# Kernel optimization log

Measured on AMD Instinct MI355X. Metric: run time of the kernel, lower is better.

## Reference

```python
import jax, jax.numpy as jnp
import numpy as np

B, S, H = 2, 2048, 2048
NH, NG = 16, 4           # attention heads, query groups
HD = H // NH             # head_dim = 128
HPG = NH // NG           # heads per group = 4


def setup_inputs() -> dict:
    key = jax.random.key(0)
    ks = jax.random.split(key, 8)
    s = 0.02
    return {
        "hidden_states": jax.random.normal(ks[0], (B, S, H), dtype=jnp.float32),
        "attention_mask": jnp.ones((B, S), dtype=jnp.int32),
        "Wq": jax.random.normal(ks[1], (H, H), dtype=jnp.float32) * s,
        "bq": jnp.zeros((H,), dtype=jnp.float32),
        "Wk": jax.random.normal(ks[2], (HD * NG, H), dtype=jnp.float32) * s,
        "bk": jnp.zeros((HD * NG,), dtype=jnp.float32),
        "Wv": jax.random.normal(ks[3], (HD * NG, H), dtype=jnp.float32) * s,
        "bv": jnp.zeros((HD * NG,), dtype=jnp.float32),
    }


def reference(hidden_states, attention_mask, Wq, bq, Wk, bk, Wv, bv):
    b, s, _ = hidden_states.shape
    scale = 1.0 / np.sqrt(HD).astype(np.float32)
    # projections (torch Linear: x @ W.T + b)
    q = hidden_states @ Wq.T + bq                      # [b,s,H]
    k = hidden_states @ Wk.T + bk                      # [b,s,NG*HD]
    v = hidden_states @ Wv.T + bv
    # q grouped so that repeat_interleave of k/v along heads == broadcast over heads_per_group
    q = q.reshape(b, s, NG, HPG, HD)                   # heads = group-major order
    k = k.reshape(b, s, NG, HD)
    v = v.reshape(b, s, NG, HD)
    scores = jnp.einsum("bsgpd,btgd->bgpst", q, k) * scale  # [b,NG,HPG,s,s]
    # mask: positions with attention_mask == 0 get finfo.min added
    mask_add = jnp.where(attention_mask == 0,
                         jnp.finfo(scores.dtype).min,
                         jnp.float32(0.0))             # [b,t]
    scores = scores + mask_add[:, None, None, None, :]
    attn = jax.nn.softmax(scores, axis=-1)             # dropout is identity in eval
    out = jnp.einsum("bgpst,btgd->bsgpd", attn, v)     # [b,s,NG,HPG,HD]
    return out.reshape(b, s, NH * HD)
```

## Files before the change

### kernel.cpp

```cpp
#include <hip/hip_runtime.h>
#include <hip/hip_bf16.h>

#define B_ 2
#define S_ 2048
#define H_ 2048
#define NH_ 16
#define NG_ 4
#define HD_ 128
#define HPG_ 4

typedef __attribute__((ext_vector_type(8))) short short8;
typedef __attribute__((ext_vector_type(4))) short short4v;
typedef __attribute__((ext_vector_type(4))) float float4v;

#define MFMA_BF16 __builtin_amdgcn_mfma_f32_16x16x32_bf16

#if __has_builtin(__builtin_amdgcn_exp2f)
#define EXP2(x) __builtin_amdgcn_exp2f(x)
#else
#define EXP2(x) exp2f(x)
#endif

__device__ __forceinline__ void gload16(const void* g, void* l) {
    __builtin_amdgcn_global_load_lds(
        (const __attribute__((address_space(1))) unsigned int*)g,
        (__attribute__((address_space(3))) unsigned int*)l, 16, 0, 0);
}

__device__ __forceinline__ short bf16bits(float f) {
    union { __hip_bfloat16 h; short s; } u;
    u.h = __float2bfloat16(f);
    return u.s;
}

__global__ __launch_bounds__(256) void cvt_all(const float* __restrict__ hs,
                                               const float* __restrict__ wq,
                                               const float* __restrict__ wk,
                                               const float* __restrict__ wv,
                                               const int* __restrict__ mask,
                                               __hip_bfloat16* __restrict__ o_hs,
                                               __hip_bfloat16* __restrict__ o_wq,
                                               __hip_bfloat16* __restrict__ o_wk,
                                               __hip_bfloat16* __restrict__ o_wv,
                                               float* __restrict__ o_m) {
    int i = blockIdx.x * 256 + threadIdx.x;
    if (blockIdx.x == 0) {
#pragma unroll
        for (int j = 0; j < 16; ++j) {
            int idx = threadIdx.x * 16 + j;
            o_m[idx] = mask[idx] ? 0.0f : -3.0e38f;
        }
    }
    const float* src;
    __hip_bfloat16* dst;
    int off;
    if (i < 1048576)      { src = hs; dst = o_hs; off = i; }
    else if (i < 1572864) { src = wq; dst = o_wq; off = i - 1048576; }
    else if (i < 1703936) { src = wk; dst = o_wk; off = i - 1572864; }
    else                  { src = wv; dst = o_wv; off = i - 1703936; }
    const float4* s4 = (const float4*)src;
    float4 a = s4[2 * (size_t)off];
    float4 b = s4[2 * (size_t)off + 1];
    union { short8 s; __hip_bfloat16 h[8]; } u;
    u.h[0] = __float2bfloat16(a.x); u.h[1] = __float2bfloat16(a.y);
    u.h[2] = __float2bfloat16(a.z); u.h[3] = __float2bfloat16(a.w);
    u.h[4] = __float2bfloat16(b.x); u.h[5] = __float2bfloat16(b.y);
    u.h[6] = __float2bfloat16(b.z); u.h[7] = __float2bfloat16(b.w);
    *(short8*)(dst + 8 * (size_t)off) = u.s;
}

__global__ __launch_bounds__(256) void gemm_qkv(const __hip_bfloat16* __restrict__ A,
                                                const __hip_bfloat16* __restrict__ Wq,
                                                const __hip_bfloat16* __restrict__ Wk,
                                                const __hip_bfloat16* __restrict__ Wv,
                                                const float* __restrict__ bq,
                                                const float* __restrict__ bk,
                                                const float* __restrict__ bv,
                                                __hip_bfloat16* __restrict__ qO,
                                                __hip_bfloat16* __restrict__ kO,
                                                __hip_bfloat16* __restrict__ vTO) {
    __shared__ char lds[32768];

    const int bx = blockIdx.x;
    const __hip_bfloat16* Bw;
    const float* bias;
    int bn, mode;
    if (bx < 16)      { Bw = Wq; bias = bq; bn = bx * 128;        mode = 0; }
    else if (bx < 20) { Bw = Wk; bias = bk; bn = (bx - 16) * 128; mode = 1; }
    else              { Bw = Wv; bias = bv; bn = (bx - 20) * 128; mode = 2; }

    const int tid = threadIdx.x;
    const int lane = tid & 63;
    const int x = lane & 15, g = lane >> 4;
    const int wid = tid >> 6;
    const int wm = wid >> 1, wn = wid & 1;
    const int bm = blockIdx.y * 128;
    const int K = 2048;

    const int srow = tid >> 2;
    const int schunk = (tid & 3) ^ ((tid >> 3) & 3);
    const __hip_bfloat16* gA0 = A + (size_t)(bm + srow) * K + schunk * 8;
    const __hip_bfloat16* gA1 = A + (size_t)(bm + 64 + srow) * K + schunk * 8;
    const __hip_bfloat16* gB0 = Bw + (size_t)(bn + srow) * K + schunk * 8;
    const __hip_bfloat16* gB1 = Bw + (size_t)(bn + 64 + srow) * K + schunk * 8;

    int aoff[4], boff[4];
    const int key = (x >> 1) & 3;
#pragma unroll
    for (int t = 0; t < 4; ++t) {
        aoff[t] = ((wm * 64 + t * 16 + x) * 32 + (g ^ key) * 8) * 2;
        boff[t] = 8192 + ((wn * 64 + t * 16 + x) * 32 + (g ^ key) * 8) * 2;
    }

    float4v acc[4][4];
#pragma unroll
    for (int i = 0; i < 4; ++i)
#pragma unroll
        for (int j = 0; j < 4; ++j) acc[i][j] = (float4v)0.f;

    gload16(gA0, lds + tid * 16);
    gload16(gA1, lds + tid * 16 + 4096);
    gload16(gB0, lds + 8192 + tid * 16);
    gload16(gB1, lds + 8192 + tid * 16 + 4096);
    gA0 += 32; gA1 += 32; gB0 += 32; gB1 += 32;

    for (int it = 0; it < 64; ++it) {
        char* cur = lds + (it & 1) * 16384;
        char* nxt = lds + ((it & 1) ^ 1) * 16384;
        __syncthreads();
        if (it < 63) {
            gload16(gA0, nxt + tid * 16);
            gload16(gA1, nxt + tid * 16 + 4096);
            gload16(gB0, nxt + 8192 + tid * 16);
            gload16(gB1, nxt + 8192 + tid * 16 + 4096);
            gA0 += 32; gA1 += 32; gB0 += 32; gB1 += 32;
        }
        short8 af[4], bf[4];
#pragma unroll
        for (int t = 0; t < 4; ++t) {
            af[t] = *(const short8*)(cur + aoff[t]);
            bf[t] = *(const short8*)(cur + boff[t]);
        }
#pragma unroll
        for (int mb = 0; mb < 4; ++mb)
#pragma unroll
            for (int nb = 0; nb < 4; ++nb)
                acc[mb][nb] = MFMA_BF16(af[mb], bf[nb], acc[mb][nb], 0, 0, 0);
    }

    if (mode <= 1) {
        const int N = (mode == 0) ? 2048 : 512;
        __hip_bfloat16* C = (mode == 0) ? qO : kO;
#pragma unroll
        for (int nb = 0; nb < 4; ++nb) {
            const int n = bn + wn * 64 + nb * 16 + x;
            const float bsv = bias[n];
#pragma unroll
            for (int mb = 0; mb < 4; ++mb) {
                const int m0 = bm + wm * 64 + mb * 16 + g * 4;
#pragma unroll
                for (int r = 0; r < 4; ++r)
                    C[(size_t)(m0 + r) * N + n] = __float2bfloat16(acc[mb][nb][r] + bsv);
            }
        }
    } else {
#pragma unroll
        for (int nb = 0; nb < 4; ++nb) {
            const int n = bn + wn * 64 + nb * 16 + x;
            const float bsv = bias[n];
            const int gv = n >> 7, d = n & 127;
#pragma unroll
            for (int mb = 0; mb < 4; ++mb) {
                const int m0 = bm + wm * 64 + mb * 16 + g * 4;
                const int bb = m0 >> 11, s = m0 & 2047;
                short4v pk;
#pragma unroll
                for (int r = 0; r < 4; ++r) pk[r] = bf16bits(acc[mb][nb][r] + bsv);
                *(short4v*)(vTO + ((size_t)(bb * NG_ + gv) * HD_ + d) * S_ + s) = pk;
            }
        }
    }
}

__global__ __launch_bounds__(256, 2) void attn(const __hip_bfloat16* __restrict__ q,
                                               const __hip_bfloat16* __restrict__ k,
                                               const __hip_bfloat16* __restrict__ vT,
                                               const float* __restrict__ M,
                                               float* __restrict__ out) {
    __shared__ char smem[50176];
    char* Ks = smem;
    char* Vs = smem + 16384;
    char* Ps = smem + 32768;

    const int tid = threadIdx.x;
    const int lane = tid & 63;
    const int w = tid >> 6;
    const int wm = w >> 1, wn = w & 1;
    const int x = lane & 15, g = lane >> 4;

    const int bid0 = blockIdx.x;
    const int bid = ((bid0 & 7) << 6) | (bid0 >> 3);
    const int qt = bid & 15;
    const int hp = (bid >> 4) & 3;
    const int gi = (bid >> 6) & 3;
    const int b = bid >> 8;
    const int head = gi * HPG_ + hp;
    const int q0 = qt * 128;

    short8 qf[4][4];
#pragma unroll
    for (int nb = 0; nb < 4; ++nb) {
        const int qq = q0 + wn * 64 + nb * 16 + x;
        const __hip_bfloat16* qrow = q + ((size_t)(b * S_ + qq) * NH_ + head) * HD_ + g * 8;
#pragma unroll
        for (int ks = 0; ks < 4; ++ks)
            qf[nb][ks] = *(const short8*)(qrow + ks * 32);
    }

    const int krow = tid >> 4;
    const int kchunk = (tid & 15) ^ krow;
    const __hip_bfloat16* kp = k + ((size_t)(b * S_ + krow) * NG_ + gi) * HD_ + kchunk * 8;
    const int vrow = tid >> 3;
    const int vchunk = (tid & 7) ^ (vrow & 7);
    const __hip_bfloat16* vp = vT + ((size_t)(b * NG_ + gi) * HD_ + vrow) * S_ + vchunk * 8;
    const float* mp = M + b * S_ + wm * 32 + g * 4;

    float4v O[4][4];
#pragma unroll
    for (int i = 0; i < 4; ++i)
#pragma unroll
        for (int j = 0; j < 4; ++j) O[i][j] = (float4v)0.f;
    float l_part[4] = {0.f, 0.f, 0.f, 0.f};

    const float SM = 0.08838834764831845f * 1.4426950408889634f;

#pragma unroll
    for (int qq = 0; qq < 4; ++qq)
        gload16(kp + qq * 8192, Ks + tid * 16 + qq * 4096);
    kp += 32768;

    for (int it = 0; it < 32; ++it) {
        __syncthreads();
        float4 mv0 = *(const float4*)(mp);
        float4 mv1 = *(const float4*)(mp + 16);
        mp += 64;
#pragma unroll
        for (int qq = 0; qq < 4; ++qq)
            gload16(vp + (size_t)qq * 65536, Vs + tid * 16 + qq * 4096);
        vp += 64;

        float4v sc[2][4];
#pragma unroll
        for (int i = 0; i < 2; ++i)
#pragma unroll
            for (int j = 0; j < 4; ++j) sc[i][j] = (float4v)0.f;
        __builtin_amdgcn_s_setprio(1);
#pragma unroll
        for (int ks = 0; ks < 4; ++ks) {
            short8 af0 = *(const short8*)(Ks + (wm * 32 + x) * 256 + (((ks * 4 + g) ^ x) * 16));
            short8 af1 = *(const short8*)(Ks + (wm * 32 + 16 + x) * 256 + (((ks * 4 + g) ^ x) * 16));
#pragma unroll
            for (int nb = 0; nb < 4; ++nb) {
                sc[0][nb] = MFMA_BF16(af0, qf[nb][ks], sc[0][nb], 0, 0, 0);
                sc[1][nb] = MFMA_BF16(af1, qf[nb][ks], sc[1][nb], 0, 0, 0);
            }
        }
        __builtin_amdgcn_s_setprio(0);

#pragma unroll
        for (int mb = 0; mb < 2; ++mb) {
            const float4 mv = mb ? mv1 : mv0;
            const int hs = wm * 8 + mb * 4 + g;
#pragma unroll
            for (int nb = 0; nb < 4; ++nb) {
                float p0 = EXP2(fmaf(sc[mb][nb][0], SM, mv.x));
                float p1 = EXP2(fmaf(sc[mb][nb][1], SM, mv.y));
                float p2 = EXP2(fmaf(sc[mb][nb][2], SM, mv.z));
                float p3 = EXP2(fmaf(sc[mb][nb][3], SM, mv.w));
                l_part[nb] += (p0 + p1) + (p2 + p3);
                short4v pk;
                pk[0] = bf16bits(p0); pk[1] = bf16bits(p1);
                pk[2] = bf16bits(p2); pk[3] = bf16bits(p3);
                *(short4v*)(Ps + (wn * 64 + nb * 16 + x) * 136 + hs * 8) = pk;
            }
        }

        __syncthreads();
        if (it < 31) {
#pragma unroll
            for (int qq = 0; qq < 4; ++qq)
                gload16(kp + qq * 8192, Ks + tid * 16 + qq * 4096);
            kp += 32768;
        }

#pragma unroll
        for (int ks = 0; ks < 2; ++ks) {
            short8 vf[4], pf[4];
#pragma unroll
            for (int i4 = 0; i4 < 4; ++i4) {
                vf[i4] = *(const short8*)(Vs + (wm * 64 + i4 * 16 + x) * 128 +
                                          (((ks * 4 + g) ^ (x & 7)) * 16));
                const char* pb = Ps + (wn * 64 + i4 * 16 + x) * 136 + (8 * ks + 2 * g) * 8;
                union { short4v h[2]; short8 s8; } uu;
                uu.h[0] = *(const short4v*)pb;
                uu.h[1] = *(const short4v*)(pb + 8);
                pf[i4] = uu.s8;
            }
            __builtin_amdgcn_s_setprio(1);
#pragma unroll
            for (int mb = 0; mb < 4; ++mb)
#pragma unroll
                for (int nb = 0; nb < 4; ++nb)
                    O[mb][nb] = MFMA_BF16(vf[mb], pf[nb], O[mb][nb], 0, 0, 0);
            __builtin_amdgcn_s_setprio(0);
        }
    }

    __syncthreads();
#pragma unroll
    for (int nb = 0; nb < 4; ++nb) {
        l_part[nb] += __shfl_xor(l_part[nb], 16);
        l_part[nb] += __shfl_xor(l_part[nb], 32);
    }
    float* lws = (float*)Ps;
    if (g == 0) {
#pragma unroll
        for (int nb = 0; nb < 4; ++nb)
            lws[wm * 128 + wn * 64 + nb * 16 + x] = l_part[nb];
    }
    __syncthreads();
    float inv[4];
#pragma unroll
    for (int nb = 0; nb < 4; ++nb)
        inv[nb] = 1.0f / (l_part[nb] + lws[(wm ^ 1) * 128 + wn * 64 + nb * 16 + x]);

#pragma unroll
    for (int mb = 0; mb < 4; ++mb) {
#pragma unroll
        for (int nb = 0; nb < 4; ++nb) {
            const int qq = q0 + wn * 64 + nb * 16 + x;
            const int d0 = wm * 64 + mb * 16 + g * 4;
            float4v o = O[mb][nb] * inv[nb];
            *(float4v*)(out + (size_t)(b * S_ + qq) * H_ + head * HD_ + d0) = o;
        }
    }
}

extern "C" void kernel_launch(void* const* d_in, const int* in_sizes, int n_in,
                              void* d_out, int out_size, void* d_ws, size_t ws_size,
                              hipStream_t stream) {
    (void)in_sizes; (void)n_in; (void)out_size; (void)ws_size;
    const float* hs = (const float*)d_in[0];
    const int* amask = (const int*)d_in[1];
    const float* Wq = (const float*)d_in[2];
    const float* bq = (const float*)d_in[3];
    const float* Wk = (const float*)d_in[4];
    const float* bk = (const float*)d_in[5];
    const float* Wv = (const float*)d_in[6];
    const float* bv = (const float*)d_in[7];
    float* out = (float*)d_out;

    char* ws = (char*)d_ws;
    __hip_bfloat16* hsB = (__hip_bfloat16*)(ws);
    __hip_bfloat16* WqB = (__hip_bfloat16*)(ws + 16777216);
    __hip_bfloat16* WkB = (__hip_bfloat16*)(ws + 25165824);
    __hip_bfloat16* WvB = (__hip_bfloat16*)(ws + 27262976);
    __hip_bfloat16* qB  = (__hip_bfloat16*)(ws + 29360128);
    __hip_bfloat16* kB  = (__hip_bfloat16*)(ws + 46137344);
    __hip_bfloat16* vTB = (__hip_bfloat16*)(ws + 50331648);
    float* Mf           = (float*)(ws + 54525952);

    cvt_all<<<7168, 256, 0, stream>>>(hs, Wq, Wk, Wv, amask, hsB, WqB, WkB, WvB, Mf);
    gemm_qkv<<<dim3(24, 32), 256, 0, stream>>>(hsB, WqB, WkB, WvB, bq, bk, bv, qB, kB, vTB);
    attn<<<512, 256, 0, stream>>>(qB, kB, vTB, Mf, out);
}
```

Baseline: 247.8 us.

## Rewrite QKV GEMM with 256x192 tiles, 4-stage LDS pipeline and concatenated weights

Replaces the 128x128 three-way QKV GEMM with one kernel that treats Wq/Wk/Wv as a single concatenated weight matrix (relying on their contiguous workspace layout) and uses 256x192 tiles on 512 threads. It adds a 4-stage global_load_lds ring buffer with split A/B loads, explicit vmcnt waits, barriers and setprio around the MFMA bursts, plus a swizzled block ordering for L2 reuse. Biases are concatenated in the conversion kernel. The aim is more arithmetic reuse per loaded tile and better overlap of loads with MFMA. In exchange it needs 112KB of dynamic LDS, which limits occupancy, and the hand-placed waitcnt makes correctness fragile.

```diff
diff --git a/kernel.cpp b/kernel.cpp
--- a/kernel.cpp
+++ b/kernel.cpp
@@ -38,17 +38,29 @@
                                                const float* __restrict__ wk,
                                                const float* __restrict__ wv,
                                                const int* __restrict__ mask,
+                                               const float* __restrict__ bq,
+                                               const float* __restrict__ bk,
+                                               const float* __restrict__ bv,
                                                __hip_bfloat16* __restrict__ o_hs,
                                                __hip_bfloat16* __restrict__ o_wq,
                                                __hip_bfloat16* __restrict__ o_wk,
                                                __hip_bfloat16* __restrict__ o_wv,
-                                               float* __restrict__ o_m) {
+                                               float* __restrict__ o_m,
+                                               float* __restrict__ o_bc) {
     int i = blockIdx.x * 256 + threadIdx.x;
     if (blockIdx.x == 0) {
 #pragma unroll
         for (int j = 0; j < 16; ++j) {
             int idx = threadIdx.x * 16 + j;
             o_m[idx] = mask[idx] ? 0.0f : -3.0e38f;
+        }
+    }
+    if (blockIdx.x == 1) {
+#pragma unroll
+        for (int j = 0; j < 12; ++j) {
+            int idx = j * 256 + threadIdx.x;
+            float v = (idx < 2048) ? bq[idx] : (idx < 2560) ? bk[idx - 2048] : bv[idx - 2560];
+            o_bc[idx] = v;
         }
     }
     const float* src;
@@ -69,114 +81,140 @@
     *(short8*)(dst + 8 * (size_t)off) = u.s;
 }
 
-__global__ __launch_bounds__(256) void gemm_qkv(const __hip_bfloat16* __restrict__ A,
-                                                const __hip_bfloat16* __restrict__ Wq,
-                                                const __hip_bfloat16* __restrict__ Wk,
-                                                const __hip_bfloat16* __restrict__ Wv,
-                                                const float* __restrict__ bq,
-                                                const float* __restrict__ bk,
-                                                const float* __restrict__ bv,
-                                                __hip_bfloat16* __restrict__ qO,
-                                                __hip_bfloat16* __restrict__ kO,
-                                                __hip_bfloat16* __restrict__ vTO) {
-    __shared__ char lds[32768];
-
-    const int bx = blockIdx.x;
-    const __hip_bfloat16* Bw;
-    const float* bias;
-    int bn, mode;
-    if (bx < 16)      { Bw = Wq; bias = bq; bn = bx * 128;        mode = 0; }
-    else if (bx < 20) { Bw = Wk; bias = bk; bn = (bx - 16) * 128; mode = 1; }
-    else              { Bw = Wv; bias = bv; bn = (bx - 20) * 128; mode = 2; }
+__global__ __launch_bounds__(512, 2) void gemm_qkv3(const __hip_bfloat16* __restrict__ A,
+                                                    const __hip_bfloat16* __restrict__ Wcat,
+                                                    const float* __restrict__ biasC,
+                                                    __hip_bfloat16* __restrict__ qO,
+                                                    __hip_bfloat16* __restrict__ kO,
+                                                    __hip_bfloat16* __restrict__ vTO) {
+    extern __shared__ char lds[];
 
     const int tid = threadIdx.x;
     const int lane = tid & 63;
     const int x = lane & 15, g = lane >> 4;
     const int wid = tid >> 6;
-    const int wm = wid >> 1, wn = wid & 1;
-    const int bm = blockIdx.y * 128;
+    const int wm = wid >> 2, wn = wid & 3;
+
+    const int id0 = blockIdx.x;
+    const int id = ((id0 & 7) << 5) | (id0 >> 3);
+    const int bn_t = id >> 4, bm_t = id & 15;
+    const int bm = bm_t * 256, bn = bn_t * 192;
     const int K = 2048;
 
     const int srow = tid >> 2;
     const int schunk = (tid & 3) ^ ((tid >> 3) & 3);
     const __hip_bfloat16* gA0 = A + (size_t)(bm + srow) * K + schunk * 8;
-    const __hip_bfloat16* gA1 = A + (size_t)(bm + 64 + srow) * K + schunk * 8;
-    const __hip_bfloat16* gB0 = Bw + (size_t)(bn + srow) * K + schunk * 8;
-    const __hip_bfloat16* gB1 = Bw + (size_t)(bn + 64 + srow) * K + schunk * 8;
-
-    int aoff[4], boff[4];
-    const int key = (x >> 1) & 3;
-#pragma unroll
-    for (int t = 0; t < 4; ++t) {
-        aoff[t] = ((wm * 64 + t * 16 + x) * 32 + (g ^ key) * 8) * 2;
-        boff[t] = 8192 + ((wn * 64 + t * 16 + x) * 32 + (g ^ key) * 8) * 2;
-    }
-
-    float4v acc[4][4];
-#pragma unroll
-    for (int i = 0; i < 4; ++i)
-#pragma unroll
-        for (int j = 0; j < 4; ++j) acc[i][j] = (float4v)0.f;
-
-    gload16(gA0, lds + tid * 16);
-    gload16(gA1, lds + tid * 16 + 4096);
-    gload16(gB0, lds + 8192 + tid * 16);
-    gload16(gB1, lds + 8192 + tid * 16 + 4096);
-    gA0 += 32; gA1 += 32; gB0 += 32; gB1 += 32;
-
-    for (int it = 0; it < 64; ++it) {
-        char* cur = lds + (it & 1) * 16384;
-        char* nxt = lds + ((it & 1) ^ 1) * 16384;
-        __syncthreads();
-        if (it < 63) {
-            gload16(gA0, nxt + tid * 16);
-            gload16(gA1, nxt + tid * 16 + 4096);
-            gload16(gB0, nxt + 8192 + tid * 16);
-            gload16(gB1, nxt + 8192 + tid * 16 + 4096);
-            gA0 += 32; gA1 += 32; gB0 += 32; gB1 += 32;
-        }
-        short8 af[4], bf[4];
-#pragma unroll
-        for (int t = 0; t < 4; ++t) {
-            af[t] = *(const short8*)(cur + aoff[t]);
-            bf[t] = *(const short8*)(cur + boff[t]);
-        }
+    const __hip_bfloat16* gA1 = A + (size_t)(bm + 128 + srow) * K + schunk * 8;
+    const __hip_bfloat16* gB0 = Wcat + (size_t)(bn + srow) * K + schunk * 8;
+    const __hip_bfloat16* gB1 = Wcat + (size_t)(bn + 128 + srow) * K + schunk * 8;
+    const bool doB1 = (tid < 256);
+
+    const int xk = (x >> 1) & 3;
+    int aoffA[8], boffB[3];
+#pragma unroll
+    for (int mb = 0; mb < 8; ++mb)
+        aoffA[mb] = (wm * 128 + mb * 16 + x) * 64 + ((g ^ xk) * 16);
+#pragma unroll
+    for (int nb = 0; nb < 3; ++nb)
+        boffB[nb] = 16384 + (wn * 48 + nb * 16 + x) * 64 + ((g ^ xk) * 16);
+
+    float4v acc[8][3];
+#pragma unroll
+    for (int i = 0; i < 8; ++i)
+#pragma unroll
+        for (int j = 0; j < 3; ++j) acc[i][j] = (float4v)0.f;
+
+#pragma unroll
+    for (int p = 0; p < 2; ++p) {
+        char* stg = lds + p * 28672;
+        gload16(gA0, stg + tid * 16);
+        gload16(gA1, stg + 8192 + tid * 16);
+        gload16(gB0, stg + 16384 + tid * 16);
+        if (doB1) gload16(gB1, stg + 24576 + tid * 16);
+        gA0 += 32; gA1 += 32; gB0 += 32; gB1 += 32;
+    }
+    if (doB1) asm volatile("s_waitcnt vmcnt(4)" ::: "memory");
+    else      asm volatile("s_waitcnt vmcnt(3)" ::: "memory");
+    __builtin_amdgcn_s_barrier();
+
+#pragma unroll 4
+    for (int t = 0; t < 64; ++t) {
+        const char* bc = lds + (t & 3) * 28672;
+        char* stg = lds + ((t + 2) & 3) * 28672;
+
+        short8 afA[4], bfr[3];
+#pragma unroll
+        for (int mb = 0; mb < 4; ++mb) afA[mb] = *(const short8*)(bc + aoffA[mb]);
+#pragma unroll
+        for (int nb = 0; nb < 3; ++nb) bfr[nb] = *(const short8*)(bc + boffB[nb]);
+        if (t < 62) {
+            gload16(gA0, stg + tid * 16);
+            gload16(gA1, stg + 8192 + tid * 16);
+            gA0 += 32; gA1 += 32;
+        }
+        __builtin_amdgcn_s_barrier();
+        asm volatile("s_waitcnt lgkmcnt(0)");
+        __builtin_amdgcn_sched_barrier(0);
+        __builtin_amdgcn_s_setprio(1);
 #pragma unroll
         for (int mb = 0; mb < 4; ++mb)
 #pragma unroll
-            for (int nb = 0; nb < 4; ++nb)
-                acc[mb][nb] = MFMA_BF16(af[mb], bf[nb], acc[mb][nb], 0, 0, 0);
-    }
-
-    if (mode <= 1) {
-        const int N = (mode == 0) ? 2048 : 512;
-        __hip_bfloat16* C = (mode == 0) ? qO : kO;
-#pragma unroll
-        for (int nb = 0; nb < 4; ++nb) {
-            const int n = bn + wn * 64 + nb * 16 + x;
-            const float bsv = bias[n];
-#pragma unroll
-            for (int mb = 0; mb < 4; ++mb) {
-                const int m0 = bm + wm * 64 + mb * 16 + g * 4;
+            for (int nb = 0; nb < 3; ++nb)
+                acc[mb][nb] = MFMA_BF16(afA[mb], bfr[nb], acc[mb][nb], 0, 0, 0);
+        __builtin_amdgcn_s_setprio(0);
+        __builtin_amdgcn_s_barrier();
+
+        short8 afB[4];
+#pragma unroll
+        for (int mb = 0; mb < 4; ++mb) afB[mb] = *(const short8*)(bc + aoffA[4 + mb]);
+        if (t < 62) {
+            gload16(gB0, stg + 16384 + tid * 16);
+            if (doB1) gload16(gB1, stg + 24576 + tid * 16);
+            gB0 += 32; gB1 += 32;
+        }
+        __builtin_amdgcn_s_barrier();
+        asm volatile("s_waitcnt lgkmcnt(0)");
+        __builtin_amdgcn_sched_barrier(0);
+        __builtin_amdgcn_s_setprio(1);
+#pragma unroll
+        for (int mb = 0; mb < 4; ++mb)
+#pragma unroll
+            for (int nb = 0; nb < 3; ++nb)
+                acc[4 + mb][nb] = MFMA_BF16(afB[mb], bfr[nb], acc[4 + mb][nb], 0, 0, 0);
+        __builtin_amdgcn_s_setprio(0);
+        if (t < 62) {
+            if (doB1) asm volatile("s_waitcnt vmcnt(4)" ::: "memory");
+            else      asm volatile("s_waitcnt vmcnt(3)" ::: "memory");
+        } else {
+            asm volatile("s_waitcnt vmcnt(0)" ::: "memory");
+        }
+        __builtin_amdgcn_s_barrier();
+    }
+
+#pragma unroll
+    for (int mb = 0; mb < 8; ++mb) {
+#pragma unroll
+        for (int nb = 0; nb < 3; ++nb) {
+            const int n = bn + wn * 48 + nb * 16 + x;
+            const float bsv = biasC[n];
+            const int m0 = bm + wm * 128 + mb * 16 + g * 4;
+            if (n < 2048) {
 #pragma unroll
                 for (int r = 0; r < 4; ++r)
-                    C[(size_t)(m0 + r) * N + n] = __float2bfloat16(acc[mb][nb][r] + bsv);
-            }
-        }
-    } else {
-#pragma unroll
-        for (int nb = 0; nb < 4; ++nb) {
-            const int n = bn + wn * 64 + nb * 16 + x;
-            const float bsv = bias[n];
-            const int gv = n >> 7, d = n & 127;
-#pragma unroll
-            for (int mb = 0; mb < 4; ++mb) {
-                const int m0 = bm + wm * 64 + mb * 16 + g * 4;
-                const int bb = m0 >> 11, s = m0 & 2047;
+                    qO[(size_t)(m0 + r) * 2048 + n] = __float2bfloat16(acc[mb][nb][r] + bsv);
+            } else if (n < 2560) {
+                const int nk = n - 2048;
+#pragma unroll
+                for (int r = 0; r < 4; ++r)
+                    kO[(size_t)(m0 + r) * 512 + nk] = __float2bfloat16(acc[mb][nb][r] + bsv);
+            } else {
+                const int nv = n - 2560;
+                const int gv = nv >> 7, d = nv & 127;
+                const int bb2 = m0 >> 11, s = m0 & 2047;
                 short4v pk;
 #pragma unroll
                 for (int r = 0; r < 4; ++r) pk[r] = bf16bits(acc[mb][nb][r] + bsv);
-                *(short4v*)(vTO + ((size_t)(bb * NG_ + gv) * HD_ + d) * S_ + s) = pk;
+                *(short4v*)(vTO + ((size_t)(bb2 * NG_ + gv) * HD_ + d) * S_ + s) = pk;
             }
         }
     }
@@ -369,8 +407,13 @@
     __hip_bfloat16* kB  = (__hip_bfloat16*)(ws + 46137344);
     __hip_bfloat16* vTB = (__hip_bfloat16*)(ws + 50331648);
     float* Mf           = (float*)(ws + 54525952);
-
-    cvt_all<<<7168, 256, 0, stream>>>(hs, Wq, Wk, Wv, amask, hsB, WqB, WkB, WvB, Mf);
-    gemm_qkv<<<dim3(24, 32), 256, 0, stream>>>(hsB, WqB, WkB, WvB, bq, bk, bv, qB, kB, vTB);
+    float* biasC        = (float*)(ws + 54542336);
+
+    hipFuncSetAttribute((const void*)gemm_qkv3,
+                        hipFuncAttributeMaxDynamicSharedMemorySize, 114688);
+
+    cvt_all<<<7168, 256, 0, stream>>>(hs, Wq, Wk, Wv, amask, bq, bk, bv,
+                                      hsB, WqB, WkB, WvB, Mf, biasC);
+    gemm_qkv3<<<256, 512, 114688, stream>>>(hsB, WqB, biasC, qB, kB, vTB);
     attn<<<512, 256, 0, stream>>>(qB, kB, vTB, Mf, out);
 }
```

Result: faster. 231.1 us (-6.7%).
